# Kernel optimization log

Measured on AMD Instinct MI355X. Metric: run time of the kernel, lower is better.

## Reference

```python
import jax, jax.numpy as jnp
import numpy as np

B, S, D, H = 4, 4096, 2048, 16
DH = D // H
SCALE = float(np.sqrt(DH))


def setup_inputs() -> dict:
    key = jax.random.key(0)
    ks = jax.random.split(key, 11)
    std = 1.0 / np.sqrt(D)
    inp = {
        "query": jax.random.normal(ks[0], (B, S, D), jnp.float32),
        "key": jax.random.normal(ks[1], (B, S, D), jnp.float32),
        "value": jax.random.normal(ks[2], (B, S, D), jnp.float32),
        "Wq": jax.random.normal(ks[3], (D, D), jnp.float32) * std,
        "bq": jax.random.normal(ks[4], (D,), jnp.float32) * std,
        "Wk": jax.random.normal(ks[5], (D, D), jnp.float32) * std,
        "bk": jax.random.normal(ks[6], (D,), jnp.float32) * std,
        "Wv": jax.random.normal(ks[7], (D, D), jnp.float32) * std,
        "bv": jax.random.normal(ks[8], (D,), jnp.float32) * std,
        "Wo": jax.random.normal(ks[9], (D, D), jnp.float32) * std,
        "bo": jax.random.normal(ks[10], (D,), jnp.float32) * std,
    }
    return inp


def reference(query, key, value, Wq, bq, Wk, bk, Wv, bv, Wo, bo):
    # Linear projections (torch nn.Linear: x @ W^T + b)
    Q = query @ Wq.T + bq          # [B,S,D]
    K = key @ Wk.T + bk
    V = value @ Wv.T + bv
    Q = Q.reshape(B, S, H, DH)
    K = K.reshape(B, S, H, DH)
    V = V.reshape(B, S, H, DH)
    # NOTE: original torch code does NOT transpose heads to dim 1, so the
    # matmul contracts over head-dim pairs at each position: scores [B,S,H,H]
    scores = jnp.einsum('bsid,bsjd->bsij', Q, K) / SCALE
    attention = jax.nn.softmax(scores, axis=-1)   # softmax over heads (faithful)
    x = jnp.einsum('bsij,bsjd->bsid', attention, V)  # [B,S,H,DH]
    # permute(0,2,1,3) -> [B,H,S,DH], then view(B,-1,D) -> [B,S,D]
    x = jnp.transpose(x, (0, 2, 1, 3)).reshape(B, S, D)
    out = x @ Wo.T + bo
    return out, attention
```

## Files before the change

kernel.cpp:

```cpp
#include <hip/hip_runtime.h>


#define DEV __device__ __forceinline__

using short8  = __attribute__((ext_vector_type(8))) short;
using ushort8 = __attribute__((ext_vector_type(8))) unsigned short;
using f32x4   = __attribute__((ext_vector_type(4))) float;
using u16x8   = __attribute__((ext_vector_type(8))) unsigned short;

constexpr int BATCH = 4, SEQ = 4096, DIM = 2048;
constexpr int GM = BATCH * SEQ;
constexpr int GN = DIM, GK = DIM;

DEV unsigned short f2bf(float f) {
  unsigned int u = __builtin_bit_cast(unsigned int, f);
  u += 0x7FFFu + ((u >> 16) & 1u);
  return (unsigned short)(u >> 16);
}
DEV float bf2f(unsigned short h) {
  unsigned int u = ((unsigned int)h) << 16;
  return __builtin_bit_cast(float, u);
}

DEV void gload16(const void* g, void* l) {
  __builtin_amdgcn_global_load_lds(
      (const __attribute__((address_space(1))) void*)g,
      (__attribute__((address_space(3))) void*)l, 16, 0, 0);
}

#define BAR    __builtin_amdgcn_s_barrier()
#define LGKM0  asm volatile("s_waitcnt lgkmcnt(0)" ::: "memory")
#define VMCNT4 asm volatile("s_waitcnt vmcnt(4)" ::: "memory")
#define SCHED0 __builtin_amdgcn_sched_barrier(0)

__global__ void cvt_f32_bf16(const float* __restrict__ src,
                             unsigned short* __restrict__ dst, int n) {
  int i = (blockIdx.x * blockDim.x + threadIdx.x) * 4;
  if (i >= n) return;
  f32x4 f = *(const f32x4*)(src + i);
  ushort4 o;
  o.x = f2bf(f[0]); o.y = f2bf(f[1]); o.z = f2bf(f[2]); o.w = f2bf(f[3]);
  *(ushort4*)(dst + i) = o;
}

template <bool OUTF32>
__global__ __launch_bounds__(512)
void gemm256(const unsigned short* __restrict__ Ap,
             const unsigned short* __restrict__ Bp,
             const float* __restrict__ bias, void* __restrict__ Cp) {
  constexpr int BK = 64, KT = GK / BK;
  __shared__ unsigned short As[2][256 * BK];
  __shared__ unsigned short Bs[2][256 * BK];

  const int tid  = threadIdx.x;
  const int lane = tid & 63;
  const int wv   = tid >> 6;
  const int wm   = wv >> 2, wn = wv & 3;

  int bid = (int)blockIdx.x;
  int swz = (bid & 7) * 64 + (bid >> 3);
  const int mt = swz & 63, nt = swz >> 6;
  const int bm0 = mt * 256, bn0 = nt * 256;

  int dstoff[4];
  size_t offA[4], offB[4];
#pragma unroll
  for (int r = 0; r < 4; ++r) {
    int d = tid * 16 + r * 8192;
    int s = d ^ (((d >> 7) & 7) << 4);
    int row = s >> 7, col = (s & 127) >> 1;
    dstoff[r] = d;
    offA[r] = (size_t)(bm0 + row) * GK + col;
    offB[r] = (size_t)(bn0 + row) * GK + col;
  }

  const int r16 = lane & 15, kb = (lane >> 4) * 16;
  const int arow = wm * 128 + r16;
  const int brow = wn * 64 + r16;

  f32x4 acc[8][4] = {};
  short8 af[4][2], bl[2][2], bh[2][2];

  auto stA = [&](int buf, int kt, int r) {
    gload16(Ap + offA[r] + (size_t)kt * BK, (char*)&As[buf][0] + dstoff[r]);
  };
  auto stB = [&](int buf, int kt, int r) {
    gload16(Bp + offB[r] + (size_t)kt * BK, (char*)&Bs[buf][0] + dstoff[r]);
  };
  auto ldf = [&](const unsigned short* base, int row, int ks) -> short8 {
    int a = (row * 128 + ks * 64 + kb) ^ ((row & 7) << 4);
    return *(const short8*)((const char*)base + a);
  };

#pragma unroll
  for (int r = 0; r < 4; ++r) stA(0, 0, r);
#pragma unroll
  for (int r = 0; r < 4; ++r) stB(0, 0, r);
#pragma unroll
  for (int r = 0; r < 4; ++r) stA(1, 1, r);
  VMCNT4;
  BAR;

  for (int kt = 0; kt < KT; ++kt) {
    const int cb = kt & 1, nb = cb ^ 1;
    const unsigned short* Ab = &As[cb][0];
    const unsigned short* Bb = &Bs[cb][0];

#pragma unroll
    for (int m = 0; m < 4; ++m) {
      af[m][0] = ldf(Ab, arow + m * 16, 0);
      af[m][1] = ldf(Ab, arow + m * 16, 1);
    }
#pragma unroll
    for (int n = 0; n < 2; ++n) {
      bl[n][0] = ldf(Bb, brow + n * 16, 0);
      bl[n][1] = ldf(Bb, brow + n * 16, 1);
    }
    if (kt + 1 < KT) { stB(nb, kt + 1, 0); stB(nb, kt + 1, 1); }
    BAR; LGKM0; SCHED0;
    __builtin_amdgcn_s_setprio(1);
#pragma unroll
    for (int m = 0; m < 4; ++m)
#pragma unroll
      for (int n = 0; n < 2; ++n) {
        acc[m][n] = __builtin_amdgcn_mfma_f32_16x16x32_bf16(af[m][0], bl[n][0], acc[m][n], 0, 0, 0);
        acc[m][n] = __builtin_amdgcn_mfma_f32_16x16x32_bf16(af[m][1], bl[n][1], acc[m][n], 0, 0, 0);
      }
    __builtin_amdgcn_s_setprio(0);
    BAR;

#pragma unroll
    for (int n = 0; n < 2; ++n) {
      bh[n][0] = ldf(Bb, brow + 32 + n * 16, 0);
      bh[n][1] = ldf(Bb, brow + 32 + n * 16, 1);
    }
    if (kt + 1 < KT) { stB(nb, kt + 1, 2); stB(nb, kt + 1, 3); }
    BAR; LGKM0; SCHED0;
    __builtin_amdgcn_s_setprio(1);
#pragma unroll
    for (int m = 0; m < 4; ++m)
#pragma unroll
      for (int n = 0; n < 2; ++n) {
        acc[m][2 + n] = __builtin_amdgcn_mfma_f32_16x16x32_bf16(af[m][0], bh[n][0], acc[m][2 + n], 0, 0, 0);
        acc[m][2 + n] = __builtin_amdgcn_mfma_f32_16x16x32_bf16(af[m][1], bh[n][1], acc[m][2 + n], 0, 0, 0);
      }
    __builtin_amdgcn_s_setprio(0);
    BAR;

#pragma unroll
    for (int m = 0; m < 4; ++m) {
      af[m][0] = ldf(Ab, arow + 64 + m * 16, 0);
      af[m][1] = ldf(Ab, arow + 64 + m * 16, 1);
    }
    if (kt + 2 < KT) { stA(cb, kt + 2, 0); stA(cb, kt + 2, 2); }
    BAR; LGKM0; SCHED0;
    __builtin_amdgcn_s_setprio(1);
#pragma unroll
    for (int m = 0; m < 4; ++m)
#pragma unroll
      for (int n = 0; n < 2; ++n) {
        acc[4 + m][2 + n] = __builtin_amdgcn_mfma_f32_16x16x32_bf16(af[m][0], bh[n][0], acc[4 + m][2 + n], 0, 0, 0);
        acc[4 + m][2 + n] = __builtin_amdgcn_mfma_f32_16x16x32_bf16(af[m][1], bh[n][1], acc[4 + m][2 + n], 0, 0, 0);
      }
    __builtin_amdgcn_s_setprio(0);
    BAR;

    if (kt + 2 < KT) { stA(cb, kt + 2, 1); stA(cb, kt + 2, 3); }
    VMCNT4;
    BAR;
    __builtin_amdgcn_s_setprio(1);
#pragma unroll
    for (int m = 0; m < 4; ++m)
#pragma unroll
      for (int n = 0; n < 2; ++n) {
        acc[4 + m][n] = __builtin_amdgcn_mfma_f32_16x16x32_bf16(af[m][0], bl[n][0], acc[4 + m][n], 0, 0, 0);
        acc[4 + m][n] = __builtin_amdgcn_mfma_f32_16x16x32_bf16(af[m][1], bl[n][1], acc[4 + m][n], 0, 0, 0);
      }
    __builtin_amdgcn_s_setprio(0);
    BAR;
  }

  float bs[4];
#pragma unroll
  for (int n = 0; n < 4; ++n) bs[n] = bias[bn0 + wn * 64 + n * 16 + r16];
  const int rb = (lane >> 4) * 4;
#pragma unroll
  for (int m = 0; m < 8; ++m)
#pragma unroll
    for (int i = 0; i < 4; ++i) {
      const size_t row = (size_t)bm0 + wm * 128 + m * 16 + rb + i;
#pragma unroll
      for (int n = 0; n < 4; ++n) {
        const int col = bn0 + wn * 64 + n * 16 + r16;
        float v = acc[m][n][i] + bs[n];
        if constexpr (OUTF32)
          ((float*)Cp)[row * GN + col] = v;
        else
          ((unsigned short*)Cp)[row * GN + col] = f2bf(v);
      }
    }
}

template <bool AF32, bool OUTF32>
__global__ __launch_bounds__(256)
void gemm_bt(const void* __restrict__ Ap, const unsigned short* __restrict__ Bp,
             const float* __restrict__ bias, void* __restrict__ Cp) {
  constexpr int BM = 128, BN = 128, BK = 32;
  __shared__ unsigned short As[BM * BK];
  __shared__ unsigned short Bs[BN * BK];

  const int tid  = threadIdx.x;
  const int lane = tid & 63;
  const int wv   = tid >> 6;

  constexpr int NWG = (GM / BM) * (GN / BN);
  int bid = (int)blockIdx.x;
  bid = (bid & 7) * (NWG >> 3) + (bid >> 3);
  const int mt = bid >> 4;
  const int nt = bid & 15;
  const int bm0 = mt * BM, bn0 = nt * BN;

  const int wr = wv >> 1, wc = wv & 1;
  const int r16 = lane & 15, kblk = lane >> 4;

  f32x4 acc[4][4] = {};

  const int srow = lane >> 2;
  const int scol = (lane & 3) * 8;

  for (int k0 = 0; k0 < GK; k0 += BK) {
    if (k0) __syncthreads();
#pragma unroll
    for (int c = 0; c < 2; ++c) {
      const int chunk = wv * 2 + c;
      const unsigned short* g =
          Bp + (size_t)(bn0 + chunk * 16 + srow) * GK + (k0 + scol);
      gload16(g, &Bs[chunk * 512]);
    }
    if constexpr (AF32) {
      const float* Af = (const float*)Ap;
      const int arow = tid >> 1;
      const int ak = (tid & 1) * 16;
      const f32x4* g4 = (const f32x4*)(Af + (size_t)(bm0 + arow) * GK + k0 + ak);
      f32x4 f[4];
      f[0] = g4[0]; f[1] = g4[1]; f[2] = g4[2]; f[3] = g4[3];
      ushort8 p0, p1;
#pragma unroll
      for (int j = 0; j < 8; ++j) {
        p0[j] = f2bf(f[j >> 2][j & 3]);
        p1[j] = f2bf(f[2 + (j >> 2)][j & 3]);
      }
      *(ushort8*)&As[arow * BK + ak]     = p0;
      *(ushort8*)&As[arow * BK + ak + 8] = p1;
    } else {
#pragma unroll
      for (int c = 0; c < 2; ++c) {
        const int chunk = wv * 2 + c;
        const unsigned short* g = (const unsigned short*)Ap +
            (size_t)(bm0 + chunk * 16 + srow) * GK + (k0 + scol);
        gload16(g, &As[chunk * 512]);
      }
    }
    __syncthreads();
    short8 a_f[4], b_f[4];
#pragma unroll
    for (int m = 0; m < 4; ++m)
      a_f[m] = *(const short8*)&As[(wr * 64 + m * 16 + r16) * BK + kblk * 8];
#pragma unroll
    for (int n = 0; n < 4; ++n)
      b_f[n] = *(const short8*)&Bs[(wc * 64 + n * 16 + r16) * BK + kblk * 8];
#pragma unroll
    for (int m = 0; m < 4; ++m)
#pragma unroll
      for (int n = 0; n < 4; ++n)
        acc[m][n] = __builtin_amdgcn_mfma_f32_16x16x32_bf16(a_f[m], b_f[n],
                                                            acc[m][n], 0, 0, 0);
  }
  const int rb = (lane >> 4) * 4;
#pragma unroll
  for (int m = 0; m < 4; ++m)
#pragma unroll
    for (int i = 0; i < 4; ++i) {
      const size_t row = bm0 + wr * 64 + m * 16 + rb + i;
#pragma unroll
      for (int n = 0; n < 4; ++n) {
        const int col = bn0 + wc * 64 + n * 16 + r16;
        float v = acc[m][n][i] + bias[col];
        if constexpr (OUTF32)
          ((float*)Cp)[row * GN + col] = v;
        else
          ((unsigned short*)Cp)[row * GN + col] = f2bf(v);
      }
    }
}

__global__ __launch_bounds__(256)
void attn_kernel(const unsigned short* __restrict__ Qb,
                 const unsigned short* __restrict__ Kb,
                 const unsigned short* __restrict__ Vb,
                 float* __restrict__ attnOut,
                 unsigned short* __restrict__ X2) {
  __shared__ float qf[16 * 128];
  __shared__ float kf[16 * 132];
  __shared__ float vf[16 * 128];
  __shared__ float sc[256];

  const int t = threadIdx.x;
  const int p = blockIdx.x;
  const size_t rowoff = (size_t)p * DIM;

  {
    const int e = t * 8;
    u16x8 qv = *(const u16x8*)(Qb + rowoff + e);
    u16x8 kv = *(const u16x8*)(Kb + rowoff + e);
    u16x8 vv = *(const u16x8*)(Vb + rowoff + e);
    const int r = t >> 4, c = (t & 15) * 8;
#pragma unroll
    for (int j = 0; j < 8; ++j) qf[r * 128 + c + j] = bf2f(qv[j]);
#pragma unroll
    for (int j = 0; j < 8; ++j) kf[r * 132 + c + j] = bf2f(kv[j]);
#pragma unroll
    for (int j = 0; j < 8; ++j) vf[r * 128 + c + j] = bf2f(vv[j]);
  }
  __syncthreads();

  const int i = t >> 4, j = t & 15;
  float s = 0.f;
#pragma unroll
  for (int d4 = 0; d4 < 32; ++d4) {
    f32x4 q4 = *(const f32x4*)&qf[i * 128 + d4 * 4];
    f32x4 k4 = *(const f32x4*)&kf[j * 132 + d4 * 4];
    s = fmaf(q4[0], k4[0], fmaf(q4[1], k4[1], fmaf(q4[2], k4[2], fmaf(q4[3], k4[3], s))));
  }
  s *= 0.08838834764831845f;

  float mx = s;
#pragma unroll
  for (int off = 8; off; off >>= 1) mx = fmaxf(mx, __shfl_xor(mx, off, 16));
  float ex = __expf(s - mx);
  float sum = ex;
#pragma unroll
  for (int off = 8; off; off >>= 1) sum += __shfl_xor(sum, off, 16);
  float a = ex / sum;

  attnOut[(size_t)p * 256 + t] = a;
  sc[t] = a;
  __syncthreads();

  const int dh0 = j * 8;
  float o[8] = {};
#pragma unroll
  for (int jj = 0; jj < 16; ++jj) {
    float aij = sc[i * 16 + jj];
#pragma unroll
    for (int e2 = 0; e2 < 8; ++e2)
      o[e2] = fmaf(aij, vf[jj * 128 + dh0 + e2], o[e2]);
  }
  const int b = p >> 12, spos = p & 4095;
  const int row = i * 256 + (spos >> 4);
  const int col = ((spos & 15) << 7) + dh0;
  ushort8 pk;
#pragma unroll
  for (int e2 = 0; e2 < 8; ++e2) pk[e2] = f2bf(o[e2]);
  *(ushort8*)(X2 + (size_t)b * (SEQ * DIM) + (size_t)row * DIM + col) = pk;
}

extern "C" void kernel_launch(void* const* d_in, const int* in_sizes, int n_in,
                              void* d_out, int out_size, void* d_ws,
                              size_t ws_size, hipStream_t stream) {
  const float* q  = (const float*)d_in[0];
  const float* k  = (const float*)d_in[1];
  const float* v  = (const float*)d_in[2];
  const float* Wq = (const float*)d_in[3];
  const float* bq = (const float*)d_in[4];
  const float* Wk = (const float*)d_in[5];
  const float* bk = (const float*)d_in[6];
  const float* Wv = (const float*)d_in[7];
  const float* bv = (const float*)d_in[8];
  const float* Wo = (const float*)d_in[9];
  const float* bo = (const float*)d_in[10];

  const size_t NE = (size_t)GM * GK;
  const size_t WE = (size_t)GK * GN;

  unsigned short* ws16 = (unsigned short*)d_ws;
  unsigned short* Wq_b = ws16;
  unsigned short* Wk_b = Wq_b + WE;
  unsigned short* Wv_b = Wk_b + WE;
  unsigned short* Wo_b = Wv_b + WE;
  unsigned short* Qb   = Wo_b + WE;
  unsigned short* Kb   = Qb + NE;
  unsigned short* Vb   = Kb + NE;
  unsigned short* X2   = Vb + NE;
  unsigned short* Qin  = X2 + NE;
  unsigned short* Kin  = Qin + NE;
  unsigned short* Vin  = Kin + NE;

  const size_t need_small = (4 * WE + 4 * NE) * 2;
  const size_t need_big   = need_small + 3 * NE * 2;
  const bool big = ws_size >= need_big;

  float* outMain = (float*)d_out;
  float* attnOut = outMain + (size_t)GM * GN;

  cvt_f32_bf16<<<WE / 1024, 256, 0, stream>>>(Wq, Wq_b, (int)WE);
  cvt_f32_bf16<<<WE / 1024, 256, 0, stream>>>(Wk, Wk_b, (int)WE);
  cvt_f32_bf16<<<WE / 1024, 256, 0, stream>>>(Wv, Wv_b, (int)WE);
  cvt_f32_bf16<<<WE / 1024, 256, 0, stream>>>(Wo, Wo_b, (int)WE);

  constexpr int G256 = (GM / 256) * (GN / 256);
  constexpr int G128 = (GM / 128) * (GN / 128);

  if (big) {
    cvt_f32_bf16<<<NE / 1024, 256, 0, stream>>>(q, Qin, (int)NE);
    cvt_f32_bf16<<<NE / 1024, 256, 0, stream>>>(k, Kin, (int)NE);
    cvt_f32_bf16<<<NE / 1024, 256, 0, stream>>>(v, Vin, (int)NE);
    gemm256<false><<<G256, 512, 0, stream>>>(Qin, Wq_b, bq, Qb);
    gemm256<false><<<G256, 512, 0, stream>>>(Kin, Wk_b, bk, Kb);
    gemm256<false><<<G256, 512, 0, stream>>>(Vin, Wv_b, bv, Vb);
  } else {
    gemm_bt<true, false><<<G128, 256, 0, stream>>>(q, Wq_b, bq, Qb);
    gemm_bt<true, false><<<G128, 256, 0, stream>>>(k, Wk_b, bk, Kb);
    gemm_bt<true, false><<<G128, 256, 0, stream>>>(v, Wv_b, bv, Vb);
  }

  attn_kernel<<<GM, 256, 0, stream>>>(Qb, Kb, Vb, attnOut, X2);

  gemm256<true><<<G256, 512, 0, stream>>>(X2, Wo_b, bo, outMain);
}
```

Before: 827.9 us.

## Fuse fp32-to-bf16 input conversion into 256-tile GEMM loads for QKV projections

The QKV projection GEMMs now read fp32 activations directly into registers, convert them to bf16 and write them to LDS inside the 256x256 pipelined GEMM. This removes the three separate conversion kernels and their bf16 intermediate buffers, saving a full write and reread of the inputs. The change also switches to 32-bit offsets, splits the LDS fragment waits with partial lgkmcnt, adds launch_bounds occupancy 2, and uses a new XCD-aware tile swizzle. Register-staged A loads add VGPR pressure and synchronous waits that may reduce overlap compared with the direct-to-LDS loads.

```diff
diff --git a/kernel.cpp b/kernel.cpp
--- a/kernel.cpp
+++ b/kernel.cpp
@@ -28,10 +28,12 @@
       (__attribute__((address_space(3))) void*)l, 16, 0, 0);
 }
 
-#define BAR    __builtin_amdgcn_s_barrier()
-#define LGKM0  asm volatile("s_waitcnt lgkmcnt(0)" ::: "memory")
-#define VMCNT4 asm volatile("s_waitcnt vmcnt(4)" ::: "memory")
-#define SCHED0 __builtin_amdgcn_sched_barrier(0)
+#define BAR      __builtin_amdgcn_s_barrier()
+#define LGKM0    asm volatile("s_waitcnt lgkmcnt(0)" ::: "memory")
+#define LGKM(N)  asm volatile("s_waitcnt lgkmcnt(" #N ")" ::: "memory")
+#define VMC(N)   asm volatile("s_waitcnt vmcnt(" #N ")" ::: "memory")
+#define SCHED0   __builtin_amdgcn_sched_barrier(0)
+#define MFMA16(a, b, c) __builtin_amdgcn_mfma_f32_16x16x32_bf16(a, b, c, 0, 0, 0)
 
 __global__ void cvt_f32_bf16(const float* __restrict__ src,
                              unsigned short* __restrict__ dst, int n) {
@@ -43,35 +45,39 @@
   *(ushort4*)(dst + i) = o;
 }
 
-template <bool OUTF32>
-__global__ __launch_bounds__(512)
-void gemm256(const unsigned short* __restrict__ Ap,
+template <bool AF32, bool OUTF32>
+__global__ __launch_bounds__(512, 2)
+void gemm256(const void* __restrict__ Ap_,
              const unsigned short* __restrict__ Bp,
              const float* __restrict__ bias, void* __restrict__ Cp) {
   constexpr int BK = 64, KT = GK / BK;
   __shared__ unsigned short As[2][256 * BK];
   __shared__ unsigned short Bs[2][256 * BK];
 
+  const float* Af          = (const float*)Ap_;
+  const unsigned short* A16 = (const unsigned short*)Ap_;
+
   const int tid  = threadIdx.x;
   const int lane = tid & 63;
   const int wv   = tid >> 6;
   const int wm   = wv >> 2, wn = wv & 3;
 
   int bid = (int)blockIdx.x;
-  int swz = (bid & 7) * 64 + (bid >> 3);
-  const int mt = swz & 63, nt = swz >> 6;
+  const int xcd = bid & 7, rr = bid >> 3;
+  const int gg = rr >> 5, jj = rr & 31;
+  const int mt = xcd * 8 + gg * 4 + (jj & 3);
+  const int nt = jj >> 2;
   const int bm0 = mt * 256, bn0 = nt * 256;
 
-  int dstoff[4];
-  size_t offA[4], offB[4];
+  const int dst0 = tid * 16;
+  int offA[4], offB[4];
 #pragma unroll
   for (int r = 0; r < 4; ++r) {
-    int d = tid * 16 + r * 8192;
+    int d = dst0 + r * 8192;
     int s = d ^ (((d >> 7) & 7) << 4);
     int row = s >> 7, col = (s & 127) >> 1;
-    dstoff[r] = d;
-    offA[r] = (size_t)(bm0 + row) * GK + col;
-    offB[r] = (size_t)(bn0 + row) * GK + col;
+    offA[r] = (bm0 + row) * GK + col;
+    offB[r] = (bn0 + row) * GK + col;
   }
 
   const int r16 = lane & 15, kb = (lane >> 4) * 16;
@@ -80,101 +86,181 @@
 
   f32x4 acc[8][4] = {};
   short8 af[4][2], bl[2][2], bh[2][2];
-
-  auto stA = [&](int buf, int kt, int r) {
-    gload16(Ap + offA[r] + (size_t)kt * BK, (char*)&As[buf][0] + dstoff[r]);
+  f32x4 areg[2][2];
+
+  auto stA16 = [&](int buf, int kt, int r) {
+    gload16(A16 + (size_t)offA[r] + (size_t)kt * BK,
+            (char*)&As[buf][0] + (dst0 + r * 8192));
   };
   auto stB = [&](int buf, int kt, int r) {
-    gload16(Bp + offB[r] + (size_t)kt * BK, (char*)&Bs[buf][0] + dstoff[r]);
+    gload16(Bp + (size_t)offB[r] + (size_t)kt * BK,
+            (char*)&Bs[buf][0] + (dst0 + r * 8192));
+  };
+  auto ldA32 = [&](int kt, int r, int slot) {
+    const float* ga = Af + (size_t)offA[r] + (size_t)kt * BK;
+    areg[slot][0] = *(const f32x4*)ga;
+    areg[slot][1] = *(const f32x4*)(ga + 4);
+  };
+  auto wrA = [&](int buf, int r, int slot) {
+    ushort8 p;
+#pragma unroll
+    for (int q = 0; q < 4; ++q) {
+      p[q]     = f2bf(areg[slot][0][q]);
+      p[4 + q] = f2bf(areg[slot][1][q]);
+    }
+    *(ushort8*)((char*)&As[buf][0] + (dst0 + r * 8192)) = p;
   };
   auto ldf = [&](const unsigned short* base, int row, int ks) -> short8 {
     int a = (row * 128 + ks * 64 + kb) ^ ((row & 7) << 4);
     return *(const short8*)((const char*)base + a);
   };
 
-#pragma unroll
-  for (int r = 0; r < 4; ++r) stA(0, 0, r);
-#pragma unroll
-  for (int r = 0; r < 4; ++r) stB(0, 0, r);
-#pragma unroll
-  for (int r = 0; r < 4; ++r) stA(1, 1, r);
-  VMCNT4;
-  BAR;
+  if constexpr (AF32) {
+    f32x4 t0[4][2];
+#pragma unroll
+    for (int r = 0; r < 4; ++r) {
+      const float* ga = Af + (size_t)offA[r];
+      t0[r][0] = *(const f32x4*)ga;
+      t0[r][1] = *(const f32x4*)(ga + 4);
+    }
+    SCHED0;
+#pragma unroll
+    for (int r = 0; r < 4; ++r) stB(0, 0, r);
+    SCHED0; VMC(4); SCHED0;
+#pragma unroll
+    for (int r = 0; r < 4; ++r) {
+      ushort8 p;
+#pragma unroll
+      for (int q = 0; q < 4; ++q) {
+        p[q] = f2bf(t0[r][0][q]); p[4 + q] = f2bf(t0[r][1][q]);
+      }
+      *(ushort8*)((char*)&As[0][0] + (dst0 + r * 8192)) = p;
+    }
+    SCHED0; VMC(0); LGKM0;
+    BAR;
+  } else {
+#pragma unroll
+    for (int r = 0; r < 4; ++r) stA16(0, 0, r);
+#pragma unroll
+    for (int r = 0; r < 4; ++r) stB(0, 0, r);
+#pragma unroll
+    for (int r = 0; r < 4; ++r) stA16(1, 1, r);
+    VMC(4);
+    BAR;
+  }
 
   for (int kt = 0; kt < KT; ++kt) {
     const int cb = kt & 1, nb = cb ^ 1;
     const unsigned short* Ab = &As[cb][0];
     const unsigned short* Bb = &Bs[cb][0];
-
-#pragma unroll
-    for (int m = 0; m < 4; ++m) {
-      af[m][0] = ldf(Ab, arow + m * 16, 0);
-      af[m][1] = ldf(Ab, arow + m * 16, 1);
-    }
-#pragma unroll
-    for (int n = 0; n < 2; ++n) {
-      bl[n][0] = ldf(Bb, brow + n * 16, 0);
-      bl[n][1] = ldf(Bb, brow + n * 16, 1);
-    }
-    if (kt + 1 < KT) { stB(nb, kt + 1, 0); stB(nb, kt + 1, 1); }
-    BAR; LGKM0; SCHED0;
+    const bool more = (kt + 1 < KT);
+
+    if constexpr (AF32) {
+      if (more) {
+        ldA32(kt + 1, 0, 0); ldA32(kt + 1, 1, 1);
+        SCHED0;
+        stB(nb, kt + 1, 0); stB(nb, kt + 1, 1);
+        SCHED0;
+      }
+    } else {
+      if (more) { stB(nb, kt + 1, 0); stB(nb, kt + 1, 1); }
+    }
+#pragma unroll
+    for (int m = 0; m < 4; ++m) af[m][0] = ldf(Ab, arow + m * 16, 0);
+#pragma unroll
+    for (int n = 0; n < 2; ++n) bl[n][0] = ldf(Bb, brow + n * 16, 0);
+    SCHED0;
+#pragma unroll
+    for (int m = 0; m < 4; ++m) af[m][1] = ldf(Ab, arow + m * 16, 1);
+#pragma unroll
+    for (int n = 0; n < 2; ++n) bl[n][1] = ldf(Bb, brow + n * 16, 1);
+    BAR;
+    LGKM(6); SCHED0;
     __builtin_amdgcn_s_setprio(1);
 #pragma unroll
     for (int m = 0; m < 4; ++m)
 #pragma unroll
-      for (int n = 0; n < 2; ++n) {
-        acc[m][n] = __builtin_amdgcn_mfma_f32_16x16x32_bf16(af[m][0], bl[n][0], acc[m][n], 0, 0, 0);
-        acc[m][n] = __builtin_amdgcn_mfma_f32_16x16x32_bf16(af[m][1], bl[n][1], acc[m][n], 0, 0, 0);
-      }
+      for (int n = 0; n < 2; ++n)
+        acc[m][n] = MFMA16(af[m][0], bl[n][0], acc[m][n]);
+    LGKM0; SCHED0;
+#pragma unroll
+    for (int m = 0; m < 4; ++m)
+#pragma unroll
+      for (int n = 0; n < 2; ++n)
+        acc[m][n] = MFMA16(af[m][1], bl[n][1], acc[m][n]);
     __builtin_amdgcn_s_setprio(0);
     BAR;
 
+    if constexpr (AF32) {
+      if (more) {
+        SCHED0; VMC(2); SCHED0;
+        wrA(nb, 0, 0); wrA(nb, 1, 1);
+        ldA32(kt + 1, 2, 0); ldA32(kt + 1, 3, 1);
+        SCHED0;
+        stB(nb, kt + 1, 2); stB(nb, kt + 1, 3);
+        SCHED0;
+      }
+    } else {
+      if (more) { stB(nb, kt + 1, 2); stB(nb, kt + 1, 3); }
+    }
 #pragma unroll
     for (int n = 0; n < 2; ++n) {
       bh[n][0] = ldf(Bb, brow + 32 + n * 16, 0);
       bh[n][1] = ldf(Bb, brow + 32 + n * 16, 1);
     }
-    if (kt + 1 < KT) { stB(nb, kt + 1, 2); stB(nb, kt + 1, 3); }
-    BAR; LGKM0; SCHED0;
+    BAR;
+    LGKM0; SCHED0;
     __builtin_amdgcn_s_setprio(1);
 #pragma unroll
     for (int m = 0; m < 4; ++m)
 #pragma unroll
       for (int n = 0; n < 2; ++n) {
-        acc[m][2 + n] = __builtin_amdgcn_mfma_f32_16x16x32_bf16(af[m][0], bh[n][0], acc[m][2 + n], 0, 0, 0);
-        acc[m][2 + n] = __builtin_amdgcn_mfma_f32_16x16x32_bf16(af[m][1], bh[n][1], acc[m][2 + n], 0, 0, 0);
+        acc[m][2 + n] = MFMA16(af[m][0], bh[n][0], acc[m][2 + n]);
+        acc[m][2 + n] = MFMA16(af[m][1], bh[n][1], acc[m][2 + n]);
       }
     __builtin_amdgcn_s_setprio(0);
     BAR;
 
+    if constexpr (AF32) {
+      if (more) {
+        SCHED0; VMC(2); SCHED0;
+        wrA(nb, 2, 0); wrA(nb, 3, 1);
+      }
+    } else {
+      if (kt + 2 < KT) { stA16(cb, kt + 2, 0); stA16(cb, kt + 2, 2); }
+    }
 #pragma unroll
     for (int m = 0; m < 4; ++m) {
       af[m][0] = ldf(Ab, arow + 64 + m * 16, 0);
       af[m][1] = ldf(Ab, arow + 64 + m * 16, 1);
     }
-    if (kt + 2 < KT) { stA(cb, kt + 2, 0); stA(cb, kt + 2, 2); }
-    BAR; LGKM0; SCHED0;
+    BAR;
+    LGKM0; SCHED0;
     __builtin_amdgcn_s_setprio(1);
 #pragma unroll
     for (int m = 0; m < 4; ++m)
 #pragma unroll
       for (int n = 0; n < 2; ++n) {
-        acc[4 + m][2 + n] = __builtin_amdgcn_mfma_f32_16x16x32_bf16(af[m][0], bh[n][0], acc[4 + m][2 + n], 0, 0, 0);
-        acc[4 + m][2 + n] = __builtin_amdgcn_mfma_f32_16x16x32_bf16(af[m][1], bh[n][1], acc[4 + m][2 + n], 0, 0, 0);
+        acc[4 + m][2 + n] = MFMA16(af[m][0], bh[n][0], acc[4 + m][2 + n]);
+        acc[4 + m][2 + n] = MFMA16(af[m][1], bh[n][1], acc[4 + m][2 + n]);
       }
     __builtin_amdgcn_s_setprio(0);
     BAR;
 
-    if (kt + 2 < KT) { stA(cb, kt + 2, 1); stA(cb, kt + 2, 3); }
-    VMCNT4;
+    if constexpr (AF32) {
+      SCHED0; VMC(0); SCHED0;
+    } else {
+      if (kt + 2 < KT) { stA16(cb, kt + 2, 1); stA16(cb, kt + 2, 3); }
+      SCHED0; VMC(4); SCHED0;
+    }
     BAR;
     __builtin_amdgcn_s_setprio(1);
 #pragma unroll
     for (int m = 0; m < 4; ++m)
 #pragma unroll
       for (int n = 0; n < 2; ++n) {
-        acc[4 + m][n] = __builtin_amdgcn_mfma_f32_16x16x32_bf16(af[m][0], bl[n][0], acc[4 + m][n], 0, 0, 0);
-        acc[4 + m][n] = __builtin_amdgcn_mfma_f32_16x16x32_bf16(af[m][1], bl[n][1], acc[4 + m][n], 0, 0, 0);
+        acc[4 + m][n] = MFMA16(af[m][0], bl[n][0], acc[4 + m][n]);
+        acc[4 + m][n] = MFMA16(af[m][1], bl[n][1], acc[4 + m][n]);
       }
     __builtin_amdgcn_s_setprio(0);
     BAR;
@@ -193,99 +279,6 @@
       for (int n = 0; n < 4; ++n) {
         const int col = bn0 + wn * 64 + n * 16 + r16;
         float v = acc[m][n][i] + bs[n];
-        if constexpr (OUTF32)
-          ((float*)Cp)[row * GN + col] = v;
-        else
-          ((unsigned short*)Cp)[row * GN + col] = f2bf(v);
-      }
-    }
-}
-
-template <bool AF32, bool OUTF32>
-__global__ __launch_bounds__(256)
-void gemm_bt(const void* __restrict__ Ap, const unsigned short* __restrict__ Bp,
-             const float* __restrict__ bias, void* __restrict__ Cp) {
-  constexpr int BM = 128, BN = 128, BK = 32;
-  __shared__ unsigned short As[BM * BK];
-  __shared__ unsigned short Bs[BN * BK];
-
-  const int tid  = threadIdx.x;
-  const int lane = tid & 63;
-  const int wv   = tid >> 6;
-
-  constexpr int NWG = (GM / BM) * (GN / BN);
-  int bid = (int)blockIdx.x;
-  bid = (bid & 7) * (NWG >> 3) + (bid >> 3);
-  const int mt = bid >> 4;
-  const int nt = bid & 15;
-  const int bm0 = mt * BM, bn0 = nt * BN;
-
-  const int wr = wv >> 1, wc = wv & 1;
-  const int r16 = lane & 15, kblk = lane >> 4;
-
-  f32x4 acc[4][4] = {};
-
-  const int srow = lane >> 2;
-  const int scol = (lane & 3) * 8;
-
-  for (int k0 = 0; k0 < GK; k0 += BK) {
-    if (k0) __syncthreads();
-#pragma unroll
-    for (int c = 0; c < 2; ++c) {
-      const int chunk = wv * 2 + c;
-      const unsigned short* g =
-          Bp + (size_t)(bn0 + chunk * 16 + srow) * GK + (k0 + scol);
-      gload16(g, &Bs[chunk * 512]);
-    }
-    if constexpr (AF32) {
-      const float* Af = (const float*)Ap;
-      const int arow = tid >> 1;
-      const int ak = (tid & 1) * 16;
-      const f32x4* g4 = (const f32x4*)(Af + (size_t)(bm0 + arow) * GK + k0 + ak);
-      f32x4 f[4];
-      f[0] = g4[0]; f[1] = g4[1]; f[2] = g4[2]; f[3] = g4[3];
-      ushort8 p0, p1;
-#pragma unroll
-      for (int j = 0; j < 8; ++j) {
-        p0[j] = f2bf(f[j >> 2][j & 3]);
-        p1[j] = f2bf(f[2 + (j >> 2)][j & 3]);
-      }
-      *(ushort8*)&As[arow * BK + ak]     = p0;
-      *(ushort8*)&As[arow * BK + ak + 8] = p1;
-    } else {
-#pragma unroll
-      for (int c = 0; c < 2; ++c) {
-        const int chunk = wv * 2 + c;
-        const unsigned short* g = (const unsigned short*)Ap +
-            (size_t)(bm0 + chunk * 16 + srow) * GK + (k0 + scol);
-        gload16(g, &As[chunk * 512]);
-      }
-    }
-    __syncthreads();
-    short8 a_f[4], b_f[4];
-#pragma unroll
-    for (int m = 0; m < 4; ++m)
-      a_f[m] = *(const short8*)&As[(wr * 64 + m * 16 + r16) * BK + kblk * 8];
-#pragma unroll
-    for (int n = 0; n < 4; ++n)
-      b_f[n] = *(const short8*)&Bs[(wc * 64 + n * 16 + r16) * BK + kblk * 8];
-#pragma unroll
-    for (int m = 0; m < 4; ++m)
-#pragma unroll
-      for (int n = 0; n < 4; ++n)
-        acc[m][n] = __builtin_amdgcn_mfma_f32_16x16x32_bf16(a_f[m], b_f[n],
-                                                            acc[m][n], 0, 0, 0);
-  }
-  const int rb = (lane >> 4) * 4;
-#pragma unroll
-  for (int m = 0; m < 4; ++m)
-#pragma unroll
-    for (int i = 0; i < 4; ++i) {
-      const size_t row = bm0 + wr * 64 + m * 16 + rb + i;
-#pragma unroll
-      for (int n = 0; n < 4; ++n) {
-        const int col = bn0 + wc * 64 + n * 16 + r16;
-        float v = acc[m][n][i] + bias[col];
         if constexpr (OUTF32)
           ((float*)Cp)[row * GN + col] = v;
         else
@@ -350,11 +343,11 @@
   const int dh0 = j * 8;
   float o[8] = {};
 #pragma unroll
-  for (int jj = 0; jj < 16; ++jj) {
-    float aij = sc[i * 16 + jj];
+  for (int jjq = 0; jjq < 16; ++jjq) {
+    float aij = sc[i * 16 + jjq];
 #pragma unroll
     for (int e2 = 0; e2 < 8; ++e2)
-      o[e2] = fmaf(aij, vf[jj * 128 + dh0 + e2], o[e2]);
+      o[e2] = fmaf(aij, vf[jjq * 128 + dh0 + e2], o[e2]);
   }
   const int b = p >> 12, spos = p & 4095;
   const int row = i * 256 + (spos >> 4);
@@ -392,13 +385,6 @@
   unsigned short* Kb   = Qb + NE;
   unsigned short* Vb   = Kb + NE;
   unsigned short* X2   = Vb + NE;
-  unsigned short* Qin  = X2 + NE;
-  unsigned short* Kin  = Qin + NE;
-  unsigned short* Vin  = Kin + NE;
-
-  const size_t need_small = (4 * WE + 4 * NE) * 2;
-  const size_t need_big   = need_small + 3 * NE * 2;
-  const bool big = ws_size >= need_big;
 
   float* outMain = (float*)d_out;
   float* attnOut = outMain + (size_t)GM * GN;
@@ -409,22 +395,12 @@
   cvt_f32_bf16<<<WE / 1024, 256, 0, stream>>>(Wo, Wo_b, (int)WE);
 
   constexpr int G256 = (GM / 256) * (GN / 256);
-  constexpr int G128 = (GM / 128) * (GN / 128);
-
-  if (big) {
-    cvt_f32_bf16<<<NE / 1024, 256, 0, stream>>>(q, Qin, (int)NE);
-    cvt_f32_bf16<<<NE / 1024, 256, 0, stream>>>(k, Kin, (int)NE);
-    cvt_f32_bf16<<<NE / 1024, 256, 0, stream>>>(v, Vin, (int)NE);
-    gemm256<false><<<G256, 512, 0, stream>>>(Qin, Wq_b, bq, Qb);
-    gemm256<false><<<G256, 512, 0, stream>>>(Kin, Wk_b, bk, Kb);
-    gemm256<false><<<G256, 512, 0, stream>>>(Vin, Wv_b, bv, Vb);
-  } else {
-    gemm_bt<true, false><<<G128, 256, 0, stream>>>(q, Wq_b, bq, Qb);
-    gemm_bt<true, false><<<G128, 256, 0, stream>>>(k, Wk_b, bk, Kb);
-    gemm_bt<true, false><<<G128, 256, 0, stream>>>(v, Wv_b, bv, Vb);
-  }
+
+  gemm256<true, false><<<G256, 512, 0, stream>>>(q, Wq_b, bq, Qb);
+  gemm256<true, false><<<G256, 512, 0, stream>>>(k, Wk_b, bk, Kb);
+  gemm256<true, false><<<G256, 512, 0, stream>>>(v, Wv_b, bv, Vb);
 
   attn_kernel<<<GM, 256, 0, stream>>>(Qb, Kb, Vb, attnOut, X2);
 
-  gemm256<true><<<G256, 512, 0, stream>>>(X2, Wo_b, bo, outMain);
-}
+  gemm256<false, true><<<G256, 512, 0, stream>>>(X2, Wo_b, bo, outMain);
+}
```

New measurement: 1.073 ms. 29.7% more time.
